# Performance work log

Hardware: AMD Instinct MI355X
Metric: run time of the kernel (lower is better)

## Reference

```python
import jax, jax.numpy as jnp
import numpy as np

B, N = 8192, 128
ALPHA, BETA = 0.5, 0.5
SIGMA1 = 0.01  # prior diagonal variance used in the temporal KL term


def setup_inputs() -> dict:
    key = jax.random.key(0)
    k1, k2, k3, k4, k5 = jax.random.split(key, 5)
    y = jax.random.normal(k1, (B, N), dtype=jnp.float32)
    mu = jax.random.normal(k2, (B, N), dtype=jnp.float32)
    lmbda = jax.random.uniform(k3, (B, N), dtype=jnp.float32, minval=0.5, maxval=2.0)
    psi = 0.1 * jax.random.normal(k4, (B, N, N), dtype=jnp.float32)
    # nu must be > n + 1 so the NIW variance is positive
    nu = jax.random.uniform(k5, (B, N), dtype=jnp.float32, minval=N + 2.0, maxval=N + 12.0)
    return {"y": y, "mu": mu, "lmbda": lmbda, "psi": psi, "nu": nu}


def reference(y, mu, lmbda, psi, nu):
    n = mu.shape[-1]
    y = jnp.nan_to_num(y, nan=0.0)

    # niw_var = diagonal(exp(psi) / (lmbda*(nu-n-1))[...,None]); only the
    # diagonal of psi contributes, so extract it first (same math, less traffic).
    psi_diag = jnp.diagonal(psi, axis1=-2, axis2=-1)              # [B, n]
    niw_var = jnp.exp(psi_diag) / (lmbda * (nu - n - 1.0))        # [B, n]

    # Multivariate KL between diag-Gaussians N(y, SIGMA1*I) and N(mu, diag(niw_var)),
    # with diagonal det/inverse/trace reduced to elementwise ops.
    mu_diff = mu - y
    term_1 = jnp.sum(jnp.log(niw_var), axis=-1) - n * jnp.log(jnp.asarray(SIGMA1, niw_var.dtype))
    term_2 = jnp.sum(SIGMA1 / niw_var, axis=-1)
    term_3 = jnp.sum(mu_diff * mu_diff / niw_var, axis=-1)
    kl = 0.5 * (term_1 - n + term_2 + term_3)                     # [B]
    temporal = jnp.sum(kl)                                        # 'sum' reduction -> scalar

    # L1 evidential error term
    evidence = lmbda + nu                                         # [B, n]
    error = jnp.mean(jnp.sum(jnp.abs(y - mu) * evidence, axis=-1))

    loss = ALPHA * temporal + BETA * error
    return loss, temporal, error
```

## Files before the change

### kernel.cpp

```cpp
#include <hip/hip_runtime.h>
#include <math.h>

#define BB 8192
#define NN 128

typedef float vf2 __attribute__((ext_vector_type(2)));

constexpr int BLOCK = 256;
constexpr int EPT = 2;
constexpr int GRID = (BB * NN) / (BLOCK * EPT);

__global__ __launch_bounds__(BLOCK) void niw_reduce_kernel(
    const float* __restrict__ y, const float* __restrict__ mu,
    const float* __restrict__ lmbda, const float* __restrict__ psi,
    const float* __restrict__ nu, double* __restrict__ partials)
{
    const int t = blockIdx.x * BLOCK + threadIdx.x;
    const int e = t * EPT;
    const int b = e >> 7;
    const int j = e & 127;

    const float* prow = psi + (size_t)b * (NN * NN) + (size_t)j * (NN + 1);
    const float pd0 = __builtin_nontemporal_load(prow);
    const float pd1 = __builtin_nontemporal_load(prow + (NN + 1));

    const vf2 yv  = __builtin_nontemporal_load(reinterpret_cast<const vf2*>(y + e));
    const vf2 muv = __builtin_nontemporal_load(reinterpret_cast<const vf2*>(mu + e));
    const vf2 lmv = __builtin_nontemporal_load(reinterpret_cast<const vf2*>(lmbda + e));
    const vf2 nuv = __builtin_nontemporal_load(reinterpret_cast<const vf2*>(nu + e));

    const float pd[2] = {pd0, pd1};

    float s1 = 0.f, s2 = 0.f, s3 = 0.f, s4 = 0.f;
#pragma unroll
    for (int k = 0; k < 2; ++k) {
        float yk = yv[k];
        yk = (yk != yk) ? 0.0f : yk;
        const float d = muv[k] - yk;
        const float denom = lmv[k] * (nuv[k] - (float)(NN + 1));
        s1 += pd[k] - __logf(denom);
        const float inv_v = denom * __expf(-pd[k]);
        s2 += inv_v;
        s3 += d * d * inv_v;
        s4 += fabsf(d) * (lmv[k] + nuv[k]);
    }

#pragma unroll
    for (int off = 32; off > 0; off >>= 1) {
        s1 += __shfl_down(s1, off);
        s2 += __shfl_down(s2, off);
        s3 += __shfl_down(s3, off);
        s4 += __shfl_down(s4, off);
    }

    __shared__ float sh[4][4];
    const int wave = threadIdx.x >> 6;
    const int lane = threadIdx.x & 63;
    if (lane == 0) {
        sh[wave][0] = s1; sh[wave][1] = s2; sh[wave][2] = s3; sh[wave][3] = s4;
    }
    __syncthreads();
    if (threadIdx.x == 0) {
        double t1 = 0, t2 = 0, t3 = 0, t4 = 0;
        for (int w = 0; w < 4; ++w) {
            t1 += sh[w][0]; t2 += sh[w][1]; t3 += sh[w][2]; t4 += sh[w][3];
        }
        double* p = partials + (size_t)blockIdx.x * 4;
        p[0] = t1; p[1] = t2; p[2] = t3; p[3] = t4;
    }
}

__global__ __launch_bounds__(256) void niw_finalize_kernel(
    const double* __restrict__ partials, float* __restrict__ out)
{
    double t1 = 0, t2 = 0, t3 = 0, t4 = 0;
    for (int i = threadIdx.x; i < GRID; i += 256) {
        const double* p = partials + (size_t)i * 4;
        t1 += p[0]; t2 += p[1]; t3 += p[2]; t4 += p[3];
    }
#pragma unroll
    for (int off = 32; off > 0; off >>= 1) {
        t1 += __shfl_down(t1, off);
        t2 += __shfl_down(t2, off);
        t3 += __shfl_down(t3, off);
        t4 += __shfl_down(t4, off);
    }
    __shared__ double sh[4][4];
    const int wave = threadIdx.x >> 6;
    const int lane = threadIdx.x & 63;
    if (lane == 0) {
        sh[wave][0] = t1; sh[wave][1] = t2; sh[wave][2] = t3; sh[wave][3] = t4;
    }
    __syncthreads();
    if (threadIdx.x == 0) {
        double S1 = 0, S2 = 0, S3 = 0, S4 = 0;
        for (int w = 0; w < 4; ++w) {
            S1 += sh[w][0]; S2 += sh[w][1]; S3 += sh[w][2]; S4 += sh[w][3];
        }
        const double SIGMA1 = 0.01;
        const double n = (double)NN;
        const double Bd = (double)BB;
        const double temporal =
            0.5 * (S1 - Bd * n * log(SIGMA1) - Bd * n + SIGMA1 * S2 + S3);
        const double error = S4 / Bd;
        const double loss = 0.5 * temporal + 0.5 * error;
        out[0] = (float)loss;
        out[1] = (float)temporal;
        out[2] = (float)error;
    }
}

extern "C" void kernel_launch(void* const* d_in, const int* in_sizes, int n_in,
                              void* d_out, int out_size, void* d_ws, size_t ws_size,
                              hipStream_t stream) {
    const float* y     = (const float*)d_in[0];
    const float* mu    = (const float*)d_in[1];
    const float* lmbda = (const float*)d_in[2];
    const float* psi   = (const float*)d_in[3];
    const float* nu    = (const float*)d_in[4];
    float* out = (float*)d_out;
    double* partials = (double*)d_ws;

    niw_reduce_kernel<<<GRID, BLOCK, 0, stream>>>(y, mu, lmbda, psi, nu, partials);
    niw_finalize_kernel<<<1, 256, 0, stream>>>(partials, out);
}
```

Measured before the change: 31.58 us.

## Fuse finalize into reduce kernel via last-block atomic counter, widen to 4 elements per thread

```diff
diff --git a/kernel.cpp b/kernel.cpp
--- a/kernel.cpp
+++ b/kernel.cpp
@@ -4,16 +4,17 @@
 #define BB 8192
 #define NN 128
 
-typedef float vf2 __attribute__((ext_vector_type(2)));
+typedef float vf4 __attribute__((ext_vector_type(4)));
 
 constexpr int BLOCK = 256;
-constexpr int EPT = 2;
+constexpr int EPT = 4;
 constexpr int GRID = (BB * NN) / (BLOCK * EPT);
 
-__global__ __launch_bounds__(BLOCK) void niw_reduce_kernel(
+__global__ __launch_bounds__(BLOCK) void niw_fused_kernel(
     const float* __restrict__ y, const float* __restrict__ mu,
     const float* __restrict__ lmbda, const float* __restrict__ psi,
-    const float* __restrict__ nu, double* __restrict__ partials)
+    const float* __restrict__ nu, double* __restrict__ partials,
+    unsigned* __restrict__ counter, float* __restrict__ out)
 {
     const int t = blockIdx.x * BLOCK + threadIdx.x;
     const int e = t * EPT;
@@ -21,19 +22,20 @@
     const int j = e & 127;
 
     const float* prow = psi + (size_t)b * (NN * NN) + (size_t)j * (NN + 1);
-    const float pd0 = __builtin_nontemporal_load(prow);
-    const float pd1 = __builtin_nontemporal_load(prow + (NN + 1));
+    const float pd[4] = {
+        __builtin_nontemporal_load(prow),
+        __builtin_nontemporal_load(prow + 129),
+        __builtin_nontemporal_load(prow + 258),
+        __builtin_nontemporal_load(prow + 387)};
 
-    const vf2 yv  = __builtin_nontemporal_load(reinterpret_cast<const vf2*>(y + e));
-    const vf2 muv = __builtin_nontemporal_load(reinterpret_cast<const vf2*>(mu + e));
-    const vf2 lmv = __builtin_nontemporal_load(reinterpret_cast<const vf2*>(lmbda + e));
-    const vf2 nuv = __builtin_nontemporal_load(reinterpret_cast<const vf2*>(nu + e));
-
-    const float pd[2] = {pd0, pd1};
+    const vf4 yv  = __builtin_nontemporal_load(reinterpret_cast<const vf4*>(y + e));
+    const vf4 muv = __builtin_nontemporal_load(reinterpret_cast<const vf4*>(mu + e));
+    const vf4 lmv = __builtin_nontemporal_load(reinterpret_cast<const vf4*>(lmbda + e));
+    const vf4 nuv = __builtin_nontemporal_load(reinterpret_cast<const vf4*>(nu + e));
 
     float s1 = 0.f, s2 = 0.f, s3 = 0.f, s4 = 0.f;
 #pragma unroll
-    for (int k = 0; k < 2; ++k) {
+    for (int k = 0; k < 4; ++k) {
         float yk = yv[k];
         yk = (yk != yk) ? 0.0f : yk;
         const float d = muv[k] - yk;
@@ -54,6 +56,7 @@
     }
 
     __shared__ float sh[4][4];
+    __shared__ bool is_last;
     const int wave = threadIdx.x >> 6;
     const int lane = threadIdx.x & 63;
     if (lane == 0) {
@@ -67,14 +70,16 @@
         }
         double* p = partials + (size_t)blockIdx.x * 4;
         p[0] = t1; p[1] = t2; p[2] = t3; p[3] = t4;
+        __threadfence();
+        const unsigned prev = atomicAdd(counter, 1u);
+        is_last = (prev == (unsigned)(GRID - 1));
     }
-}
+    __syncthreads();
+    if (!is_last) return;
 
-__global__ __launch_bounds__(256) void niw_finalize_kernel(
-    const double* __restrict__ partials, float* __restrict__ out)
-{
+    __threadfence();
     double t1 = 0, t2 = 0, t3 = 0, t4 = 0;
-    for (int i = threadIdx.x; i < GRID; i += 256) {
+    for (int i = threadIdx.x; i < GRID; i += BLOCK) {
         const double* p = partials + (size_t)i * 4;
         t1 += p[0]; t2 += p[1]; t3 += p[2]; t4 += p[3];
     }
@@ -85,17 +90,15 @@
         t3 += __shfl_down(t3, off);
         t4 += __shfl_down(t4, off);
     }
-    __shared__ double sh[4][4];
-    const int wave = threadIdx.x >> 6;
-    const int lane = threadIdx.x & 63;
+    __shared__ double shd[4][4];
     if (lane == 0) {
-        sh[wave][0] = t1; sh[wave][1] = t2; sh[wave][2] = t3; sh[wave][3] = t4;
+        shd[wave][0] = t1; shd[wave][1] = t2; shd[wave][2] = t3; shd[wave][3] = t4;
     }
     __syncthreads();
     if (threadIdx.x == 0) {
         double S1 = 0, S2 = 0, S3 = 0, S4 = 0;
         for (int w = 0; w < 4; ++w) {
-            S1 += sh[w][0]; S2 += sh[w][1]; S3 += sh[w][2]; S4 += sh[w][3];
+            S1 += shd[w][0]; S2 += shd[w][1]; S3 += shd[w][2]; S4 += shd[w][3];
         }
         const double SIGMA1 = 0.01;
         const double n = (double)NN;
@@ -119,8 +122,11 @@
     const float* psi   = (const float*)d_in[3];
     const float* nu    = (const float*)d_in[4];
     float* out = (float*)d_out;
-    double* partials = (double*)d_ws;
 
-    niw_reduce_kernel<<<GRID, BLOCK, 0, stream>>>(y, mu, lmbda, psi, nu, partials);
-    niw_finalize_kernel<<<1, 256, 0, stream>>>(partials, out);
+    unsigned* counter = (unsigned*)d_ws;
+    double* partials  = (double*)((char*)d_ws + 64);
+
+    hipMemsetAsync(counter, 0, 64, stream);
+    niw_fused_kernel<<<GRID, BLOCK, 0, stream>>>(y, mu, lmbda, psi, nu,
+                                                 partials, counter, out);
 }
```

New measurement: 77.77 us. 2.46x slower.
